# Kernel optimization log

Measured on AMD Instinct MI355X. Metric: run time of the kernel, lower is better.

## Reference

```python
import jax, jax.numpy as jnp
import numpy as np

EMBED = 1024
HEADS = 16
HEAD_DIM = EMBED // HEADS
HIDDEN = 4096
EPS = 1e-5


def setup_inputs() -> dict:
    key = jax.random.key(0)
    ks = jax.random.split(key, 12)
    s = 0.02
    inp = {
        "x": jax.random.normal(ks[0], (2, 2048, EMBED), dtype=jnp.float32),
        "ln1_scale": jnp.ones((EMBED,), jnp.float32),
        "ln1_shift": jnp.zeros((EMBED,), jnp.float32),
        "ln2_scale": jnp.ones((EMBED,), jnp.float32),
        "ln2_shift": jnp.zeros((EMBED,), jnp.float32),
        "wq": jax.random.normal(ks[1], (EMBED, EMBED), jnp.float32) * s,
        "bq": jnp.zeros((EMBED,), jnp.float32),
        "wk": jax.random.normal(ks[2], (EMBED, EMBED), jnp.float32) * s,
        "bk": jnp.zeros((EMBED,), jnp.float32),
        "wv": jax.random.normal(ks[3], (EMBED, EMBED), jnp.float32) * s,
        "bv": jnp.zeros((EMBED,), jnp.float32),
        "wo": jax.random.normal(ks[4], (EMBED, EMBED), jnp.float32) * s,
        "bo": jnp.zeros((EMBED,), jnp.float32),
        "w1": jax.random.normal(ks[5], (EMBED, HIDDEN), jnp.float32) * s,
        "b1": jnp.zeros((HIDDEN,), jnp.float32),
        "w2": jax.random.normal(ks[6], (HIDDEN, EMBED), jnp.float32) * s,
        "b2": jnp.zeros((EMBED,), jnp.float32),
    }
    return inp


def _layernorm(x, scale, shift):
    mean = jnp.mean(x, axis=-1, keepdims=True)
    var = jnp.var(x, axis=-1, keepdims=True)
    return scale * (x - mean) * jax.lax.rsqrt(var + EPS) + shift


def _block(x, ln1_scale, ln1_shift, ln2_scale, ln2_shift,
           wq, bq, wk, bk, wv, bv, wo, bo, w1, b1, w2, b2):
    B, S, D = x.shape
    h = _layernorm(x, ln1_scale, ln1_shift)
    q = (h @ wq + bq).reshape(B, S, HEADS, HEAD_DIM).transpose(0, 2, 1, 3)
    k = (h @ wk + bk).reshape(B, S, HEADS, HEAD_DIM).transpose(0, 2, 1, 3)
    v = (h @ wv + bv).reshape(B, S, HEADS, HEAD_DIM).transpose(0, 2, 1, 3)
    # [B,H,S,S] eager attention scores, matching the reference exactly
    scores = jnp.einsum("bhqd,bhkd->bhqk", q, k) * (HEAD_DIM ** -0.5)
    causal = jnp.tril(jnp.ones((S, S), dtype=bool))
    scores = jnp.where(causal, scores, -jnp.inf)
    attn = jax.nn.softmax(scores, axis=-1)
    ctx = jnp.einsum("bhqk,bhkd->bhqd", attn, v)
    ctx = ctx.transpose(0, 2, 1, 3).reshape(B, S, D)
    x = x + (ctx @ wo + bo)
    h = _layernorm(x, ln2_scale, ln2_shift)
    h = jax.nn.gelu(h @ w1 + b1, approximate=False)
    x = x + (h @ w2 + b2)
    return x


def reference(x, ln1_scale, ln1_shift, ln2_scale, ln2_shift,
              wq, bq, wk, bk, wv, bv, wo, bo, w1, b1, w2, b2):
    return _block(x, ln1_scale, ln1_shift, ln2_scale, ln2_shift,
                  wq, bq, wk, bk, wv, bv, wo, bo, w1, b1, w2, b2)
```

## Files before the change

kernel.cpp:

```cpp
#include <hip/hip_runtime.h>


typedef __bf16 bf16x8_t __attribute__((ext_vector_type(8)));
typedef float f32x4_t __attribute__((ext_vector_type(4)));
typedef unsigned short u16x8 __attribute__((ext_vector_type(8)));

__device__ __forceinline__ unsigned short f2b(float f) {
    unsigned int u = __builtin_bit_cast(unsigned int, f);
    u += 0x7fffu + ((u >> 16) & 1u);
    return (unsigned short)(u >> 16);
}
__device__ __forceinline__ bf16x8_t as_bf(u16x8 v) {
    return __builtin_bit_cast(bf16x8_t, v);
}
__device__ __forceinline__ void store_out(float* p, float v) { *p = v; }
__device__ __forceinline__ void store_out(unsigned short* p, float v) { *p = f2b(v); }

__device__ __forceinline__ void glds16(const unsigned short* g, unsigned short* l) {
    __builtin_amdgcn_global_load_lds(
        (const __attribute__((address_space(1))) unsigned int*)g,
        (__attribute__((address_space(3))) unsigned int*)l, 16, 0, 0);
}

template <int N>
__device__ __forceinline__ void wait_vm() {
    asm volatile("s_waitcnt vmcnt(%0)" ::"i"(N) : "memory");
}

__global__ __launch_bounds__(256) void transpose_cast(
    const float* __restrict__ src, unsigned short* __restrict__ dst,
    int K, int N) {
    __shared__ float tile[32][33];
    const int k0 = blockIdx.x * 32, n0 = blockIdx.y * 32;
    const int c = threadIdx.x & 31, r8 = threadIdx.x >> 5;
#pragma unroll
    for (int i = 0; i < 4; i++) {
        const int r = r8 + i * 8;
        tile[r][c] = src[(size_t)(k0 + r) * N + n0 + c];
    }
    __syncthreads();
#pragma unroll
    for (int i = 0; i < 4; i++) {
        const int rr = r8 + i * 8;
        dst[(size_t)(n0 + rr) * K + k0 + c] = f2b(tile[c][rr]);
    }
}

__global__ __launch_bounds__(256) void transpose_cast4(
    const float* __restrict__ s0, const float* __restrict__ s1,
    const float* __restrict__ s2, const float* __restrict__ s3,
    unsigned short* __restrict__ wqkvt, unsigned short* __restrict__ wot) {
    __shared__ float tile[32][33];
    const int z = blockIdx.z;
    const float* src = (z == 0) ? s0 : (z == 1) ? s1 : (z == 2) ? s2 : s3;
    unsigned short* dst = (z < 3) ? wqkvt + ((size_t)z << 20) : wot;
    const int k0 = blockIdx.x * 32, n0 = blockIdx.y * 32;
    const int c = threadIdx.x & 31, r8 = threadIdx.x >> 5;
#pragma unroll
    for (int i = 0; i < 4; i++) {
        const int r = r8 + i * 8;
        tile[r][c] = src[(size_t)(k0 + r) * 1024 + n0 + c];
    }
    __syncthreads();
#pragma unroll
    for (int i = 0; i < 4; i++) {
        const int rr = r8 + i * 8;
        dst[(size_t)(n0 + rr) * 1024 + k0 + c] = f2b(tile[c][rr]);
    }
}

__global__ __launch_bounds__(256) void vtrans_kernel(
    const unsigned short* __restrict__ src, unsigned short* __restrict__ dst) {
    __shared__ unsigned short tile[32][34];
    const int s0 = blockIdx.x * 32, hd0 = blockIdx.y * 32, b = blockIdx.z;
    const int c = threadIdx.x & 31, r8 = threadIdx.x >> 5;
#pragma unroll
    for (int i = 0; i < 4; i++) {
        const int r = r8 + i * 8;
        tile[r][c] = src[(size_t)(b * 2048 + s0 + r) * 3072 + hd0 + c];
    }
    __syncthreads();
#pragma unroll
    for (int i = 0; i < 4; i++) {
        const int rr = r8 + i * 8;
        dst[(size_t)(b * 1024 + hd0 + rr) * 2048 + s0 + c] = tile[c][rr];
    }
}

__global__ __launch_bounds__(256) void ln_kernel(
    const float* __restrict__ X,
    const float* __restrict__ scale,
    const float* __restrict__ shift,
    unsigned short* __restrict__ Hout) {
    const int tok = blockIdx.x;
    const int tid = threadIdx.x;
    const size_t base = (size_t)tok * 1024 + tid * 4;
    float4 xv = *(const float4*)(X + base);
    float f[4] = {xv.x, xv.y, xv.z, xv.w};
    float s = 0.f, s2 = 0.f;
#pragma unroll
    for (int i = 0; i < 4; i++) { s += f[i]; s2 += f[i] * f[i]; }
#pragma unroll
    for (int off = 32; off >= 1; off >>= 1) {
        s += __shfl_down(s, off);
        s2 += __shfl_down(s2, off);
    }
    __shared__ float red[8];
    const int wv = tid >> 6;
    if ((tid & 63) == 0) { red[wv] = s; red[4 + wv] = s2; }
    __syncthreads();
    s = red[0] + red[1] + red[2] + red[3];
    s2 = red[4] + red[5] + red[6] + red[7];
    const float mean = s * (1.f / 1024.f);
    const float var = s2 * (1.f / 1024.f) - mean * mean;
    const float rstd = rsqrtf(var + 1e-5f);
    const float4 sc = *(const float4*)(scale + tid * 4);
    const float4 sh = *(const float4*)(shift + tid * 4);
    unsigned short ov[4];
    ov[0] = f2b((f[0] - mean) * rstd * sc.x + sh.x);
    ov[1] = f2b((f[1] - mean) * rstd * sc.y + sh.y);
    ov[2] = f2b((f[2] - mean) * rstd * sc.z + sh.z);
    ov[3] = f2b((f[3] - mean) * rstd * sc.w + sh.w);
    *(unsigned long long*)(Hout + base) = *(unsigned long long*)ov;
}

template <int BN, int EPI, typename OutT>
__global__ __launch_bounds__(256) void gemm_kernel(
    const unsigned short* __restrict__ A, const unsigned short* __restrict__ Bt,
    const float* __restrict__ bp0, const float* __restrict__ bp1,
    const float* __restrict__ bp2, const float* __restrict__ bp3,
    const float* __restrict__ res, OutT* __restrict__ C, int M, int N, int K) {
    constexpr int BSUB = BN / 16;
    constexpr int JF = BN / 32;
    __shared__ __align__(16) unsigned short As[2][8 * 512];
    __shared__ __align__(16) unsigned short Bs[2][BSUB * 512];
    const int tid = threadIdx.x;
    const int w = tid >> 6, lane = tid & 63;
    const int quad = lane >> 4, l16 = lane & 15;
    const int bm = blockIdx.x * 128, bn = blockIdx.y * BN;
    const int wm = (w & 1) * 64, wn = (w >> 1) * (BN / 2);

    f32x4_t acc[4][JF];
#pragma unroll
    for (int i = 0; i < 4; i++)
#pragma unroll
        for (int j = 0; j < JF; j++) acc[i][j] = f32x4_t{0.f, 0.f, 0.f, 0.f};

    const unsigned short* Abase = A + (size_t)(bm + l16) * K + quad * 8;
    const unsigned short* Bbase = Bt + (size_t)(bn + l16) * K + quad * 8;

    {
        for (int s = w; s < 8; s += 4)
            glds16(Abase + (size_t)s * 16 * K, &As[0][s * 512]);
        for (int s = w; s < BSUB; s += 4)
            glds16(Bbase + (size_t)s * 16 * K, &Bs[0][s * 512]);
    }
    __syncthreads();

    int buf = 0;
    for (int k0 = 0; k0 < K; k0 += 32) {
        if (k0 + 32 < K) {
            const int kn = k0 + 32;
            for (int s = w; s < 8; s += 4)
                glds16(Abase + (size_t)s * 16 * K + kn, &As[buf ^ 1][s * 512]);
            for (int s = w; s < BSUB; s += 4)
                glds16(Bbase + (size_t)s * 16 * K + kn, &Bs[buf ^ 1][s * 512]);
        }
        bf16x8_t af[4], bfv[JF];
#pragma unroll
        for (int i = 0; i < 4; i++)
            af[i] = as_bf(*(const u16x8*)&As[buf][((wm >> 4) + i) * 512 + lane * 8]);
#pragma unroll
        for (int j = 0; j < JF; j++)
            bfv[j] = as_bf(*(const u16x8*)&Bs[buf][((wn >> 4) + j) * 512 + lane * 8]);
#pragma unroll
        for (int i = 0; i < 4; i++)
#pragma unroll
            for (int j = 0; j < JF; j++)
                acc[i][j] = __builtin_amdgcn_mfma_f32_16x16x32_bf16(af[i], bfv[j], acc[i][j], 0, 0, 0);
        __syncthreads();
        buf ^= 1;
    }

#pragma unroll
    for (int i = 0; i < 4; i++) {
        const int row = bm + wm + i * 16 + quad * 4;
#pragma unroll
        for (int j = 0; j < JF; j++) {
            const int col = bn + wn + j * 16 + l16;
            const int sel = col >> 10;
            const float* bp = (sel == 0) ? bp0 : (sel == 1) ? bp1 : (sel == 2) ? bp2 : bp3;
            const float bv = bp[col & 1023];
#pragma unroll
            for (int r = 0; r < 4; r++) {
                float v = acc[i][j][r] + bv;
                if (EPI == 1) v += res[(size_t)(row + r) * N + col];
                if (EPI == 2) v = 0.5f * v * (1.f + erff(v * 0.70710678118f));
                store_out(&C[(size_t)(row + r) * N + col], v);
            }
        }
    }
}

template <int EPI, typename OutT>
__global__ __launch_bounds__(512, 2) void gemm_pipe256(
    const unsigned short* __restrict__ A, const unsigned short* __restrict__ Bt,
    const float* __restrict__ bp0, const float* __restrict__ bp1,
    const float* __restrict__ bp2, const float* __restrict__ bp3,
    OutT* __restrict__ C, int M, int N, int K) {
    constexpr int D = 3, NBUF = 4;
    __shared__ __align__(16) unsigned short As[NBUF][16 * 512];
    __shared__ __align__(16) unsigned short Bs[NBUF][16 * 512];
    const int tid = threadIdx.x;
    const int w = tid >> 6, lane = tid & 63;
    const int quad = lane >> 4, l16 = lane & 15;
    const int bm = blockIdx.x * 256, bn = blockIdx.y * 256;
    const int wm = (w & 1) * 128, wn = (w >> 1) * 64;

    f32x4_t acc[8][4];
#pragma unroll
    for (int i = 0; i < 8; i++)
#pragma unroll
        for (int j = 0; j < 4; j++) acc[i][j] = f32x4_t{0.f, 0.f, 0.f, 0.f};

    const unsigned short* Abase = A + (size_t)(bm + l16) * K + quad * 8;
    const unsigned short* Bbase = Bt + (size_t)(bn + l16) * K + quad * 8;

    auto stage = [&](int kt, int bufi) {
        const int kn = kt * 32;
        const int s0 = w * 2, s1 = w * 2 + 1;
        glds16(Abase + (size_t)s0 * 16 * K + kn, &As[bufi][s0 * 512]);
        glds16(Abase + (size_t)s1 * 16 * K + kn, &As[bufi][s1 * 512]);
        glds16(Bbase + (size_t)s0 * 16 * K + kn, &Bs[bufi][s0 * 512]);
        glds16(Bbase + (size_t)s1 * 16 * K + kn, &Bs[bufi][s1 * 512]);
    };
    auto compute = [&](int bufi) {
        bf16x8_t af[8], bfv[4];
#pragma unroll
        for (int i = 0; i < 8; i++)
            af[i] = as_bf(*(const u16x8*)&As[bufi][((wm >> 4) + i) * 512 + lane * 8]);
#pragma unroll
        for (int j = 0; j < 4; j++)
            bfv[j] = as_bf(*(const u16x8*)&Bs[bufi][((wn >> 4) + j) * 512 + lane * 8]);
#pragma unroll
        for (int i = 0; i < 8; i++)
#pragma unroll
            for (int j = 0; j < 4; j++)
                acc[i][j] = __builtin_amdgcn_mfma_f32_16x16x32_bf16(af[i], bfv[j], acc[i][j], 0, 0, 0);
    };

    const int NT = K >> 5;
#pragma unroll
    for (int t = 0; t < D; ++t) stage(t, t);

    int buf = 0, sbuf = D;
    for (int t = 0; t < NT - D; ++t) {
        wait_vm<8>();
        __builtin_amdgcn_s_barrier();
        __builtin_amdgcn_sched_barrier(0);
        stage(t + D, sbuf);
        sbuf = (sbuf + 1) & 3;
        compute(buf);
        buf = (buf + 1) & 3;
    }
    wait_vm<8>(); __builtin_amdgcn_s_barrier(); __builtin_amdgcn_sched_barrier(0);
    compute(buf); buf = (buf + 1) & 3;
    wait_vm<4>(); __builtin_amdgcn_s_barrier(); __builtin_amdgcn_sched_barrier(0);
    compute(buf); buf = (buf + 1) & 3;
    wait_vm<0>(); __builtin_amdgcn_s_barrier(); __builtin_amdgcn_sched_barrier(0);
    compute(buf);

#pragma unroll
    for (int i = 0; i < 8; i++) {
        const int row = bm + wm + i * 16 + quad * 4;
#pragma unroll
        for (int j = 0; j < 4; j++) {
            const int col = bn + wn + j * 16 + l16;
            const int sel = col >> 10;
            const float* bp = (sel == 0) ? bp0 : (sel == 1) ? bp1 : (sel == 2) ? bp2 : bp3;
            const float bv = bp[col & 1023];
#pragma unroll
            for (int r = 0; r < 4; r++) {
                float v = acc[i][j][r] + bv;
                if (EPI == 2) v = 0.5f * v * (1.f + erff(v * 0.70710678118f));
                store_out(&C[(size_t)(row + r) * N + col], v);
            }
        }
    }
}

#define LP 68

__global__ __launch_bounds__(256, 3) void attn_kernel(
    const unsigned short* __restrict__ Q, const unsigned short* __restrict__ K,
    const unsigned short* __restrict__ Vt, unsigned short* __restrict__ O,
    int ld) {
    __shared__ __align__(16) unsigned short Ks[3][8 * 512];
    __shared__ __align__(16) unsigned short Vs[3][8 * 512];
    __shared__ __align__(16) unsigned short Ps[4][32 * LP];
    const int tid = threadIdx.x;
    const int w = tid >> 6, lane = tid & 63;
    const int quad = lane >> 4, l16 = lane & 15;
    const int hh = blockIdx.x >> 1, bb = blockIdx.x & 1;
    const int y = blockIdx.y;
    const int qb = (y >= 8) ? (y - 8) : (15 - y);
    const int q0 = qb * 128;
    const int tmax = 2 * qb + 1;
    const size_t seqbase = (size_t)bb * 2048;
    const int hoff = hh * 64;
    const unsigned short* vtb = Vt + (size_t)(bb * 16 + hh) * 64 * 2048;
    const float cs = 0.18033688f;

    bf16x8_t qf[2][2];
#pragma unroll
    for (int i = 0; i < 2; i++) {
        const unsigned short* qr = Q + (seqbase + q0 + i * 64 + w * 16 + l16) * ld + hoff;
        qf[i][0] = as_bf(*(const u16x8*)(qr + quad * 8));
        qf[i][1] = as_bf(*(const u16x8*)(qr + 32 + quad * 8));
    }

    f32x4_t o[2][4];
#pragma unroll
    for (int i = 0; i < 2; i++)
#pragma unroll
        for (int jd = 0; jd < 4; jd++) o[i][jd] = f32x4_t{0.f, 0.f, 0.f, 0.f};
    float ls[2][4] = {{0.f, 0.f, 0.f, 0.f}, {0.f, 0.f, 0.f, 0.f}};

    auto stage = [&](int t, int buf) {
        for (int s = w; s < 16; s += 4) {
            if (s < 8) {
                const unsigned short* src =
                    K + (seqbase + t * 64 + (s >> 1) * 16 + l16) * ld + hoff + (s & 1) * 32 + quad * 8;
                glds16(src, &Ks[buf][s * 512]);
            } else {
                const int v = s - 8;
                const unsigned short* src =
                    vtb + (size_t)((v >> 1) * 16 + l16) * 2048 + t * 64 + (v & 1) * 32 + quad * 8;
                glds16(src, &Vs[buf][v * 512]);
            }
        }
    };

    stage(0, 0);
    stage(1, 1);

    for (int t = 0; t <= tmax; ++t) {
        if (t == tmax) wait_vm<0>(); else wait_vm<4>();
        __builtin_amdgcn_s_barrier();
        __builtin_amdgcn_sched_barrier(0);
        if (t + 2 <= tmax) stage(t + 2, (t + 2) % 3);

        const int buf = t % 3;

        bf16x8_t kf[4][2], vf[4][2];
#pragma unroll
        for (int jn = 0; jn < 4; jn++) {
            kf[jn][0] = as_bf(*(const u16x8*)&Ks[buf][(jn * 2 + 0) * 512 + lane * 8]);
            kf[jn][1] = as_bf(*(const u16x8*)&Ks[buf][(jn * 2 + 1) * 512 + lane * 8]);
            vf[jn][0] = as_bf(*(const u16x8*)&Vs[buf][(jn * 2 + 0) * 512 + lane * 8]);
            vf[jn][1] = as_bf(*(const u16x8*)&Vs[buf][(jn * 2 + 1) * 512 + lane * 8]);
        }

#pragma unroll
        for (int i = 0; i < 2; i++) {
            if (i == 0 && t > 2 * qb) continue;
            const bool diag = (t == 2 * qb + i);
#pragma unroll
            for (int jn = 0; jn < 4; jn++) {
                f32x4_t z = f32x4_t{0.f, 0.f, 0.f, 0.f};
                z = __builtin_amdgcn_mfma_f32_16x16x32_bf16(qf[i][0], kf[jn][0], z, 0, 0, 0);
                z = __builtin_amdgcn_mfma_f32_16x16x32_bf16(qf[i][1], kf[jn][1], z, 0, 0, 0);
#pragma unroll
                for (int r = 0; r < 4; r++) {
                    float p = exp2f(fminf(z[r] * cs, 60.f));
                    if (diag) {
                        const int col = t * 64 + jn * 16 + l16;
                        const int row = q0 + i * 64 + w * 16 + quad * 4 + r;
                        p = (col <= row) ? p : 0.f;
                    }
                    ls[i][r] += p;
                    Ps[w][(i * 16 + quad * 4 + r) * LP + jn * 16 + l16] = f2b(p);
                }
            }
        }

#pragma unroll
        for (int i = 0; i < 2; i++) {
            if (i == 0 && t > 2 * qb) continue;
            const bf16x8_t pf0 = as_bf(*(const u16x8*)&Ps[w][(i * 16 + l16) * LP + quad * 8]);
            const bf16x8_t pf1 = as_bf(*(const u16x8*)&Ps[w][(i * 16 + l16) * LP + 32 + quad * 8]);
#pragma unroll
            for (int jd = 0; jd < 4; jd++) {
                o[i][jd] = __builtin_amdgcn_mfma_f32_16x16x32_bf16(pf0, vf[jd][0], o[i][jd], 0, 0, 0);
                o[i][jd] = __builtin_amdgcn_mfma_f32_16x16x32_bf16(pf1, vf[jd][1], o[i][jd], 0, 0, 0);
            }
        }
    }

#pragma unroll
    for (int i = 0; i < 2; i++)
#pragma unroll
        for (int r = 0; r < 4; r++) {
            float s = ls[i][r];
            s += __shfl_xor(s, 1);
            s += __shfl_xor(s, 2);
            s += __shfl_xor(s, 4);
            s += __shfl_xor(s, 8);
            const float inv = 1.f / s;
            const size_t row = seqbase + q0 + i * 64 + w * 16 + quad * 4 + r;
#pragma unroll
            for (int jd = 0; jd < 4; jd++)
                O[row * 1024 + hoff + jd * 16 + l16] = f2b(o[i][jd][r] * inv);
        }
}

extern "C" void kernel_launch(void* const* d_in, const int* in_sizes, int n_in,
                              void* d_out, int out_size, void* d_ws, size_t ws_size,
                              hipStream_t stream) {
    const float* x = (const float*)d_in[0];
    const float* ln1s = (const float*)d_in[1];
    const float* ln1b = (const float*)d_in[2];
    const float* ln2s = (const float*)d_in[3];
    const float* ln2b = (const float*)d_in[4];
    const float* wq = (const float*)d_in[5];
    const float* bq = (const float*)d_in[6];
    const float* wk = (const float*)d_in[7];
    const float* bk = (const float*)d_in[8];
    const float* wv = (const float*)d_in[9];
    const float* bv = (const float*)d_in[10];
    const float* wo = (const float*)d_in[11];
    const float* bo = (const float*)d_in[12];
    const float* w1 = (const float*)d_in[13];
    const float* b1 = (const float*)d_in[14];
    const float* w2 = (const float*)d_in[15];
    const float* b2 = (const float*)d_in[16];
    float* out = (float*)d_out;

    char* ws = (char*)d_ws;
    const size_t MB = 1u << 20;
    unsigned short* wqkvt = (unsigned short*)(ws + 0 * MB);
    unsigned short* wot   = (unsigned short*)(ws + 6 * MB);
    unsigned short* w1t   = (unsigned short*)(ws + 8 * MB);
    unsigned short* w2t   = (unsigned short*)(ws + 16 * MB);
    unsigned short* h     = (unsigned short*)(ws + 24 * MB);
    unsigned short* vt    = (unsigned short*)(ws + 24 * MB);
    unsigned short* qkv   = (unsigned short*)(ws + 32 * MB);
    unsigned short* ctx   = (unsigned short*)(ws + 56 * MB);
    unsigned short* h2    = (unsigned short*)(ws + 24 * MB);
    float*          x1    = (float*)(ws + 64 * MB);
    unsigned short* g     = (unsigned short*)(ws + 32 * MB);

    const dim3 blk(256);

    transpose_cast4<<<dim3(32, 32, 4), blk, 0, stream>>>(wq, wk, wv, wo, wqkvt, wot);
    transpose_cast<<<dim3(32, 128), blk, 0, stream>>>(w1, w1t, 1024, 4096);
    transpose_cast<<<dim3(128, 32), blk, 0, stream>>>(w2, w2t, 4096, 1024);

    ln_kernel<<<4096, blk, 0, stream>>>(x, ln1s, ln1b, h);
    gemm_pipe256<0, unsigned short><<<dim3(16, 12), dim3(512), 0, stream>>>(
        h, wqkvt, bq, bk, bv, bv, qkv, 4096, 3072, 1024);
    vtrans_kernel<<<dim3(64, 32, 2), blk, 0, stream>>>(qkv + 2048, vt);
    attn_kernel<<<dim3(32, 16), blk, 0, stream>>>(qkv, qkv + 1024, vt, ctx, 3072);
    gemm_kernel<64, 1, float><<<dim3(32, 16), blk, 0, stream>>>(
        ctx, wot, bo, bo, bo, bo, x, x1, 4096, 1024, 1024);
    ln_kernel<<<4096, blk, 0, stream>>>(x1, ln2s, ln2b, h2);
    gemm_pipe256<2, unsigned short><<<dim3(16, 16), dim3(512), 0, stream>>>(
        h2, w1t, b1, b1 + 1024, b1 + 2048, b1 + 3072, g, 4096, 4096, 1024);
    gemm_kernel<64, 1, float><<<dim3(32, 16), blk, 0, stream>>>(
        g, w2t, b2, b2, b2, b2, x1, out, 4096, 1024, 4096);
}
```

Before: 488.8 us.

## Store GEMM operands in MFMA-tile-packed layout for contiguous LDS loads

```diff
diff --git a/kernel.cpp b/kernel.cpp
--- a/kernel.cpp
+++ b/kernel.cpp
@@ -15,6 +15,11 @@
 }
 __device__ __forceinline__ void store_out(float* p, float v) { *p = v; }
 __device__ __forceinline__ void store_out(unsigned short* p, float v) { *p = f2b(v); }
+
+__device__ __forceinline__ size_t pidx(int m, int k, int K) {
+    return (((size_t)((m >> 4) * (K >> 5) + (k >> 5))) << 9) +
+           (((k & 31) >> 3) << 7) + ((m & 15) << 3) + (k & 7);
+}
 
 __device__ __forceinline__ void glds16(const unsigned short* g, unsigned short* l) {
     __builtin_amdgcn_global_load_lds(
@@ -42,7 +47,7 @@
 #pragma unroll
     for (int i = 0; i < 4; i++) {
         const int rr = r8 + i * 8;
-        dst[(size_t)(n0 + rr) * K + k0 + c] = f2b(tile[c][rr]);
+        dst[pidx(n0 + rr, k0 + c, K)] = f2b(tile[c][rr]);
     }
 }
 
@@ -65,7 +70,7 @@
 #pragma unroll
     for (int i = 0; i < 4; i++) {
         const int rr = r8 + i * 8;
-        dst[(size_t)(n0 + rr) * 1024 + k0 + c] = f2b(tile[c][rr]);
+        dst[pidx(n0 + rr, k0 + c, 1024)] = f2b(tile[c][rr]);
     }
 }
 
@@ -83,7 +88,9 @@
 #pragma unroll
     for (int i = 0; i < 4; i++) {
         const int rr = r8 + i * 8;
-        dst[(size_t)(b * 1024 + hd0 + rr) * 2048 + s0 + c] = tile[c][rr];
+        const int g = b * 1024 + hd0 + rr;
+        const int panel = g >> 6, local = g & 63;
+        dst[((size_t)panel << 17) + pidx(local, s0 + c, 2048)] = tile[c][rr];
     }
 }
 
@@ -121,15 +128,14 @@
     ov[1] = f2b((f[1] - mean) * rstd * sc.y + sh.y);
     ov[2] = f2b((f[2] - mean) * rstd * sc.z + sh.z);
     ov[3] = f2b((f[3] - mean) * rstd * sc.w + sh.w);
-    *(unsigned long long*)(Hout + base) = *(unsigned long long*)ov;
+    *(unsigned long long*)(Hout + pidx(tok, tid * 4, 1024)) = *(unsigned long long*)ov;
 }
 
 template <int BN, int EPI, typename OutT>
 __global__ __launch_bounds__(256) void gemm_kernel(
     const unsigned short* __restrict__ A, const unsigned short* __restrict__ Bt,
-    const float* __restrict__ bp0, const float* __restrict__ bp1,
-    const float* __restrict__ bp2, const float* __restrict__ bp3,
-    const float* __restrict__ res, OutT* __restrict__ C, int M, int N, int K) {
+    const float* __restrict__ bias, const float* __restrict__ res,
+    OutT* __restrict__ C, int M, int N, int K) {
     constexpr int BSUB = BN / 16;
     constexpr int JF = BN / 32;
     __shared__ __align__(16) unsigned short As[2][8 * 512];
@@ -139,6 +145,7 @@
     const int quad = lane >> 4, l16 = lane & 15;
     const int bm = blockIdx.x * 128, bn = blockIdx.y * BN;
     const int wm = (w & 1) * 64, wn = (w >> 1) * (BN / 2);
+    const int KT = K >> 5;
 
     f32x4_t acc[4][JF];
 #pragma unroll
@@ -146,25 +153,24 @@
 #pragma unroll
         for (int j = 0; j < JF; j++) acc[i][j] = f32x4_t{0.f, 0.f, 0.f, 0.f};
 
-    const unsigned short* Abase = A + (size_t)(bm + l16) * K + quad * 8;
-    const unsigned short* Bbase = Bt + (size_t)(bn + l16) * K + quad * 8;
+    const unsigned short* Ab = A + (((size_t)(bm >> 4) * KT) << 9) + lane * 8;
+    const unsigned short* Bb = Bt + (((size_t)(bn >> 4) * KT) << 9) + lane * 8;
 
     {
         for (int s = w; s < 8; s += 4)
-            glds16(Abase + (size_t)s * 16 * K, &As[0][s * 512]);
+            glds16(Ab + ((size_t)(s * KT) << 9), &As[0][s * 512]);
         for (int s = w; s < BSUB; s += 4)
-            glds16(Bbase + (size_t)s * 16 * K, &Bs[0][s * 512]);
+            glds16(Bb + ((size_t)(s * KT) << 9), &Bs[0][s * 512]);
     }
     __syncthreads();
 
     int buf = 0;
-    for (int k0 = 0; k0 < K; k0 += 32) {
-        if (k0 + 32 < K) {
-            const int kn = k0 + 32;
+    for (int kt = 0; kt < KT; ++kt) {
+        if (kt + 1 < KT) {
             for (int s = w; s < 8; s += 4)
-                glds16(Abase + (size_t)s * 16 * K + kn, &As[buf ^ 1][s * 512]);
+                glds16(Ab + ((size_t)(s * KT + kt + 1) << 9), &As[buf ^ 1][s * 512]);
             for (int s = w; s < BSUB; s += 4)
-                glds16(Bbase + (size_t)s * 16 * K + kn, &Bs[buf ^ 1][s * 512]);
+                glds16(Bb + ((size_t)(s * KT + kt + 1) << 9), &Bs[buf ^ 1][s * 512]);
         }
         bf16x8_t af[4], bfv[JF];
 #pragma unroll
@@ -188,21 +194,18 @@
 #pragma unroll
         for (int j = 0; j < JF; j++) {
             const int col = bn + wn + j * 16 + l16;
-            const int sel = col >> 10;
-            const float* bp = (sel == 0) ? bp0 : (sel == 1) ? bp1 : (sel == 2) ? bp2 : bp3;
-            const float bv = bp[col & 1023];
+            const float bv = bias[col];
 #pragma unroll
             for (int r = 0; r < 4; r++) {
                 float v = acc[i][j][r] + bv;
                 if (EPI == 1) v += res[(size_t)(row + r) * N + col];
-                if (EPI == 2) v = 0.5f * v * (1.f + erff(v * 0.70710678118f));
                 store_out(&C[(size_t)(row + r) * N + col], v);
             }
         }
     }
 }
 
-template <int EPI, typename OutT>
+template <int EPI, bool PACKC, typename OutT>
 __global__ __launch_bounds__(512, 2) void gemm_pipe256(
     const unsigned short* __restrict__ A, const unsigned short* __restrict__ Bt,
     const float* __restrict__ bp0, const float* __restrict__ bp1,
@@ -216,6 +219,7 @@
     const int quad = lane >> 4, l16 = lane & 15;
     const int bm = blockIdx.x * 256, bn = blockIdx.y * 256;
     const int wm = (w & 1) * 128, wn = (w >> 1) * 64;
+    const int KT = K >> 5;
 
     f32x4_t acc[8][4];
 #pragma unroll
@@ -223,16 +227,15 @@
 #pragma unroll
         for (int j = 0; j < 4; j++) acc[i][j] = f32x4_t{0.f, 0.f, 0.f, 0.f};
 
-    const unsigned short* Abase = A + (size_t)(bm + l16) * K + quad * 8;
-    const unsigned short* Bbase = Bt + (size_t)(bn + l16) * K + quad * 8;
+    const unsigned short* Ab = A + (((size_t)(bm >> 4) * KT) << 9) + lane * 8;
+    const unsigned short* Bb = Bt + (((size_t)(bn >> 4) * KT) << 9) + lane * 8;
 
     auto stage = [&](int kt, int bufi) {
-        const int kn = kt * 32;
-        const int s0 = w * 2, s1 = w * 2 + 1;
-        glds16(Abase + (size_t)s0 * 16 * K + kn, &As[bufi][s0 * 512]);
-        glds16(Abase + (size_t)s1 * 16 * K + kn, &As[bufi][s1 * 512]);
-        glds16(Bbase + (size_t)s0 * 16 * K + kn, &Bs[bufi][s0 * 512]);
-        glds16(Bbase + (size_t)s1 * 16 * K + kn, &Bs[bufi][s1 * 512]);
+        const int s0 = w * 2, s1 = s0 + 1;
+        glds16(Ab + ((size_t)(s0 * KT + kt) << 9), &As[bufi][s0 * 512]);
+        glds16(Ab + ((size_t)(s1 * KT + kt) << 9), &As[bufi][s1 * 512]);
+        glds16(Bb + ((size_t)(s0 * KT + kt) << 9), &Bs[bufi][s0 * 512]);
+        glds16(Bb + ((size_t)(s1 * KT + kt) << 9), &Bs[bufi][s1 * 512]);
     };
     auto compute = [&](int bufi) {
         bf16x8_t af[8], bfv[4];
@@ -249,12 +252,11 @@
                 acc[i][j] = __builtin_amdgcn_mfma_f32_16x16x32_bf16(af[i], bfv[j], acc[i][j], 0, 0, 0);
     };
 
-    const int NT = K >> 5;
 #pragma unroll
     for (int t = 0; t < D; ++t) stage(t, t);
 
     int buf = 0, sbuf = D;
-    for (int t = 0; t < NT - D; ++t) {
+    for (int t = 0; t < KT - D; ++t) {
         wait_vm<8>();
         __builtin_amdgcn_s_barrier();
         __builtin_amdgcn_sched_barrier(0);
@@ -283,7 +285,10 @@
             for (int r = 0; r < 4; r++) {
                 float v = acc[i][j][r] + bv;
                 if (EPI == 2) v = 0.5f * v * (1.f + erff(v * 0.70710678118f));
-                store_out(&C[(size_t)(row + r) * N + col], v);
+                if constexpr (PACKC)
+                    store_out(&C[pidx(row + r, col, N)], v);
+                else
+                    store_out(&C[(size_t)(row + r) * N + col], v);
             }
         }
     }
@@ -308,7 +313,7 @@
     const int tmax = 2 * qb + 1;
     const size_t seqbase = (size_t)bb * 2048;
     const int hoff = hh * 64;
-    const unsigned short* vtb = Vt + (size_t)(bb * 16 + hh) * 64 * 2048;
+    const unsigned short* vtb = Vt + ((size_t)(bb * 16 + hh) << 17);
     const float cs = 0.18033688f;
 
     bf16x8_t qf[2][2];
@@ -335,7 +340,7 @@
             } else {
                 const int v = s - 8;
                 const unsigned short* src =
-                    vtb + (size_t)((v >> 1) * 16 + l16) * 2048 + t * 64 + (v & 1) * 32 + quad * 8;
+                    vtb + ((size_t)((v >> 1) * 64 + t * 2 + (v & 1)) << 9) + lane * 8;
                 glds16(src, &Vs[buf][v * 512]);
             }
         }
@@ -407,10 +412,10 @@
             s += __shfl_xor(s, 4);
             s += __shfl_xor(s, 8);
             const float inv = 1.f / s;
-            const size_t row = seqbase + q0 + i * 64 + w * 16 + quad * 4 + r;
+            const int row = (int)seqbase + q0 + i * 64 + w * 16 + quad * 4 + r;
 #pragma unroll
             for (int jd = 0; jd < 4; jd++)
-                O[row * 1024 + hoff + jd * 16 + l16] = f2b(o[i][jd][r] * inv);
+                O[pidx(row, hoff + jd * 16 + l16, 1024)] = f2b(o[i][jd][r] * inv);
         }
 }
 
@@ -457,15 +462,15 @@
     transpose_cast<<<dim3(128, 32), blk, 0, stream>>>(w2, w2t, 4096, 1024);
 
     ln_kernel<<<4096, blk, 0, stream>>>(x, ln1s, ln1b, h);
-    gemm_pipe256<0, unsigned short><<<dim3(16, 12), dim3(512), 0, stream>>>(
+    gemm_pipe256<0, false, unsigned short><<<dim3(16, 12), dim3(512), 0, stream>>>(
         h, wqkvt, bq, bk, bv, bv, qkv, 4096, 3072, 1024);
     vtrans_kernel<<<dim3(64, 32, 2), blk, 0, stream>>>(qkv + 2048, vt);
     attn_kernel<<<dim3(32, 16), blk, 0, stream>>>(qkv, qkv + 1024, vt, ctx, 3072);
     gemm_kernel<64, 1, float><<<dim3(32, 16), blk, 0, stream>>>(
-        ctx, wot, bo, bo, bo, bo, x, x1, 4096, 1024, 1024);
+        ctx, wot, bo, x, x1, 4096, 1024, 1024);
     ln_kernel<<<4096, blk, 0, stream>>>(x1, ln2s, ln2b, h2);
-    gemm_pipe256<2, unsigned short><<<dim3(16, 16), dim3(512), 0, stream>>>(
+    gemm_pipe256<2, true, unsigned short><<<dim3(16, 16), dim3(512), 0, stream>>>(
         h2, w1t, b1, b1 + 1024, b1 + 2048, b1 + 3072, g, 4096, 4096, 1024);
     gemm_kernel<64, 1, float><<<dim3(32, 16), blk, 0, stream>>>(
-        g, w2t, b2, b2, b2, b2, x1, out, 4096, 1024, 4096);
-}
+        g, w2t, b2, x1, out, 4096, 1024, 4096);
+}
```

Result: no change. 485.4 us (-0.7%).
